# Kernel optimization log

Measured on AMD Instinct MI355X. Metric: run time of the kernel, lower is better.

The kernel has to match this reference:

```python
import jax, jax.numpy as jnp
import numpy as np

HIDDEN = 4096
N_HEADS = 32
N_KV_HEADS = 8
HEAD_SIZE = HIDDEN // N_HEADS  # 128
ROPE_THETA = 10000.0
SEQ_LEN = 1024
BATCH = 4


def setup_inputs() -> dict:
    key = jax.random.key(0)
    k1, k2, k3 = jax.random.split(key, 3)
    scale = 1.0 / np.sqrt(HIDDEN)
    hidden_states = jax.random.normal(k1, (BATCH * SEQ_LEN, HIDDEN), dtype=jnp.float32)
    w_qkv = jax.random.normal(k2, ((N_HEADS + 2 * N_KV_HEADS) * HEAD_SIZE, HIDDEN), dtype=jnp.float32) * scale
    w_o = jax.random.normal(k3, (HIDDEN, N_HEADS * HEAD_SIZE), dtype=jnp.float32) * scale
    return {"hidden_states": hidden_states, "w_qkv": w_qkv, "w_o": w_o, "seq_len": SEQ_LEN}


def _rope(x, pos, theta):
    # x: [B, S, H, D]; pos: [S] absolute positions; rotate-half (LLAMA/NeoX) style
    d = x.shape[-1]
    inv_freq = 1.0 / (theta ** (jnp.arange(0, d, 2, dtype=jnp.float32) / d))  # [D/2]
    ang = pos.astype(jnp.float32)[:, None] * inv_freq[None, :]  # [S, D/2]
    cos = jnp.cos(ang)[None, :, None, :]
    sin = jnp.sin(ang)[None, :, None, :]
    x1, x2 = jnp.split(x, 2, axis=-1)
    return jnp.concatenate([x1 * cos - x2 * sin, x2 * cos + x1 * sin], axis=-1)


def reference(hidden_states, w_qkv, w_o, seq_len):
    total, hidden = hidden_states.shape
    B = total // seq_len
    hd = HEAD_SIZE
    # fused QKV projection (bias-free), split like the torch module
    qkv = hidden_states @ w_qkv.T  # [T, (H+2K)*hd]
    q, k, v = jnp.split(qkv, [N_HEADS * hd, (N_HEADS + N_KV_HEADS) * hd], axis=1)
    q = q.reshape(B, seq_len, N_HEADS, hd)
    k = k.reshape(B, seq_len, N_KV_HEADS, hd)
    v = v.reshape(B, seq_len, N_KV_HEADS, hd)
    # inline RoPE (ROPE_LLAMA) on q and k at absolute positions
    pos = jnp.arange(seq_len)
    q = _rope(q, pos, ROPE_THETA)
    k = _rope(k, pos, ROPE_THETA)
    # GQA: map each q head to its kv head (kv_head_mapping = repeat_interleave)
    groups = N_HEADS // N_KV_HEADS
    k = jnp.repeat(k, groups, axis=2)  # [B, S, H, hd]
    v = jnp.repeat(v, groups, axis=2)
    scale = hd ** -0.5
    scores = jnp.einsum('bqhd,bkhd->bhqk', q, k) * scale  # [B, H, S, S]
    causal = jnp.tril(jnp.ones((seq_len, seq_len), dtype=bool))
    scores = jnp.where(causal[None, None], scores, jnp.finfo(scores.dtype).min)
    probs = jax.nn.softmax(scores, axis=-1)
    attn = jnp.einsum('bhqk,bkhd->bqhd', probs, v).reshape(total, N_HEADS * hd)
    return attn @ w_o.T  # [T, hidden]
```

## Files before the change

### kernel.cpp

```cpp
#include <hip/hip_runtime.h>


typedef short bf16x8 __attribute__((ext_vector_type(8)));
typedef short bf16x4 __attribute__((ext_vector_type(4)));
typedef float floatx4 __attribute__((ext_vector_type(4)));
typedef unsigned short u16x4 __attribute__((ext_vector_type(4)));

__device__ __forceinline__ unsigned short f2bf(float f) {
  unsigned u = __float_as_uint(f);
  u += 0x7FFFu + ((u >> 16) & 1u);
  return (unsigned short)(u >> 16);
}
__device__ __forceinline__ float bf2f(unsigned short h) {
  return __uint_as_float(((unsigned)h) << 16);
}

__device__ __forceinline__ void async16(const void* g, void* l) {
  __builtin_amdgcn_global_load_lds(
      (const __attribute__((address_space(1))) unsigned int*)g,
      (__attribute__((address_space(3))) unsigned int*)l, 16, 0, 0);
}

__global__ void cvt_f32_bf16(const float4* __restrict__ in,
                             u16x4* __restrict__ out, int n4) {
  int i = blockIdx.x * 256 + threadIdx.x;
  if (i < n4) {
    float4 v = in[i];
    u16x4 o;
    o.x = f2bf(v.x); o.y = f2bf(v.y); o.z = f2bf(v.z); o.w = f2bf(v.w);
    out[i] = o;
  }
}

template <int OUT_BF16>
__global__ __launch_bounds__(512, 2) void gemm256(
    const unsigned short* __restrict__ A, const unsigned short* __restrict__ B,
    void* __restrict__ Cout, int M, int N, int K) {
  __shared__ __align__(16) unsigned short As[4][8192];
  __shared__ __align__(16) unsigned short Bs[4][8192];
  const int tid = threadIdx.x;
  const int wave = tid >> 6, lane = tid & 63;
  const int wm = wave >> 2, wn = wave & 3;
  const int l16 = lane & 15, c4 = lane >> 4;
  const int bm = blockIdx.y << 8, bn = blockIdx.x << 8;

  int afOff[8], bfOff[4];
#pragma unroll
  for (int mi = 0; mi < 8; ++mi) {
    int r = wm * 128 + mi * 16 + l16;
    int pr = r >> 1, l8 = ((r & 1) << 2) | c4;
    afOff[mi] = pr * 128 + ((l8 ^ (pr & 7)) << 4);
  }
#pragma unroll
  for (int ni = 0; ni < 4; ++ni) {
    int r = wn * 64 + ni * 16 + l16;
    int pr = r >> 1, l8 = ((r & 1) << 2) | c4;
    bfOff[ni] = pr * 128 + ((l8 ^ (pr & 7)) << 4);
  }

  const int sp = lane >> 3;
  const int l8s = (lane & 7) ^ sp;
  const int so = l8s >> 2, sc = (l8s & 3) << 3;
  const unsigned short* aS0 = A + (size_t)(bm + wave * 16 + sp * 2 + so) * K + sc;
  const unsigned short* aS1 = A + (size_t)(bm + (wave + 8) * 16 + sp * 2 + so) * K + sc;
  const unsigned short* bS0 = B + (size_t)(bn + wave * 16 + sp * 2 + so) * K + sc;
  const unsigned short* bS1 = B + (size_t)(bn + (wave + 8) * 16 + sp * 2 + so) * K + sc;
  const int dst0 = wave * 1024, dst1 = (wave + 8) * 1024;

  floatx4 acc[8][4];
#pragma unroll
  for (int mi = 0; mi < 8; ++mi)
#pragma unroll
    for (int ni = 0; ni < 4; ++ni) acc[mi][ni] = (floatx4){0.f, 0.f, 0.f, 0.f};

  const int NT = K >> 5;
  async16(aS0, (char*)As[0] + dst0);
  async16(aS1, (char*)As[0] + dst1);
  async16(bS0, (char*)Bs[0] + dst0);
  async16(bS1, (char*)Bs[0] + dst1);
  async16(aS0 + 32, (char*)As[1] + dst0);
  async16(aS1 + 32, (char*)As[1] + dst1);
  async16(bS0 + 32, (char*)Bs[1] + dst0);
  async16(bS1 + 32, (char*)Bs[1] + dst1);
  asm volatile("s_waitcnt vmcnt(4)" ::: "memory");
  __builtin_amdgcn_s_barrier();

  size_t koff = 64;
  for (int t = 0; t < NT; ++t) {
    const char* aB = (const char*)As[t & 3];
    const char* bB = (const char*)Bs[t & 3];
    char* aD = (char*)As[(t + 2) & 3];
    char* bD = (char*)Bs[(t + 2) & 3];
    const bool st = (t + 2) < NT;

    bf16x8 af[8], bf[4];
#pragma unroll
    for (int mi = 0; mi < 4; ++mi) af[mi] = *(const bf16x8*)(aB + afOff[mi]);
#pragma unroll
    for (int ni = 0; ni < 4; ++ni) bf[ni] = *(const bf16x8*)(bB + bfOff[ni]);
    if (st) { async16(aS0 + koff, aD + dst0); async16(aS1 + koff, aD + dst1); }
    __builtin_amdgcn_s_barrier();
    __builtin_amdgcn_s_setprio(1);
#pragma unroll
    for (int mi = 0; mi < 4; ++mi)
#pragma unroll
      for (int ni = 0; ni < 4; ++ni)
        acc[mi][ni] = __builtin_amdgcn_mfma_f32_16x16x32_bf16(
            af[mi], bf[ni], acc[mi][ni], 0, 0, 0);
    __builtin_amdgcn_s_setprio(0);
    __builtin_amdgcn_s_barrier();

#pragma unroll
    for (int mi = 4; mi < 8; ++mi) af[mi] = *(const bf16x8*)(aB + afOff[mi]);
    if (st) { async16(bS0 + koff, bD + dst0); async16(bS1 + koff, bD + dst1); }
    __builtin_amdgcn_s_barrier();
    __builtin_amdgcn_s_setprio(1);
#pragma unroll
    for (int mi = 4; mi < 8; ++mi)
#pragma unroll
      for (int ni = 0; ni < 4; ++ni)
        acc[mi][ni] = __builtin_amdgcn_mfma_f32_16x16x32_bf16(
            af[mi], bf[ni], acc[mi][ni], 0, 0, 0);
    __builtin_amdgcn_s_setprio(0);
    if (st) asm volatile("s_waitcnt vmcnt(4)" ::: "memory");
    else    asm volatile("s_waitcnt vmcnt(0)" ::: "memory");
    __builtin_amdgcn_s_barrier();
    koff += 32;
  }

  const int col0 = bn + wn * 64 + l16;
#pragma unroll
  for (int mi = 0; mi < 8; ++mi) {
    const int row0 = bm + wm * 128 + mi * 16 + c4 * 4;
#pragma unroll
    for (int ni = 0; ni < 4; ++ni)
#pragma unroll
      for (int r = 0; r < 4; ++r) {
        if (OUT_BF16)
          ((unsigned short*)Cout)[(size_t)(row0 + r) * N + col0 + ni * 16] =
              f2bf(acc[mi][ni][r]);
        else
          ((float*)Cout)[(size_t)(row0 + r) * N + col0 + ni * 16] =
              acc[mi][ni][r];
      }
  }
}

__global__ void rope_k_kernel(unsigned short* __restrict__ qkv) {
  const int t = blockIdx.x;
  const int s = t & 1023;
  const int head = 32 + blockIdx.y * 4 + (threadIdx.x >> 6);
  const int d = threadIdx.x & 63;
  unsigned short* p = qkv + (size_t)t * 6144 + head * 128;
  float x1 = bf2f(p[d]), x2 = bf2f(p[d + 64]);
  float inv_freq = exp2f((float)d * -0.20762050593046015f);
  float ang = (float)s * inv_freq;
  float c, sn;
  __sincosf(ang, &sn, &c);
  p[d] = f2bf(x1 * c - x2 * sn);
  p[d + 64] = f2bf(x2 * c + x1 * sn);
}

__global__ __launch_bounds__(256, 3) void flash_attn(
    const unsigned short* __restrict__ qkv, unsigned short* __restrict__ aout) {
  const int pr = blockIdx.x;
  const int h = blockIdx.y, b = blockIdx.z;
  const int kh = h >> 2;
  const int tid = threadIdx.x;
  const int wave = tid >> 6, lane = tid & 63;
  const int quad = lane >> 4, l16 = lane & 15;

  __shared__ __align__(16) unsigned short Ks[64][136];
  __shared__ __align__(16) unsigned short Vt[128][68];
  __shared__ __align__(16) unsigned short Ps[64][68];

  const int krow = tid >> 4, kcol = (tid & 15) << 3;
  const int vrb = (tid & 15) << 2, vcol = (tid >> 4) << 3;
  const unsigned short* kp = qkv + (size_t)(b << 10) * 6144 + 4096 + kh * 128;
  const unsigned short* vp = qkv + (size_t)(b << 10) * 6144 + 5120 + kh * 128;

  for (int half = 0; half < 2; ++half) {
    const int qt = half ? pr : 15 - pr;
    const int q0 = qt << 6;

    bf16x8 qf[4];
    {
      const int qrow = q0 + wave * 16 + l16;
      const unsigned short* qp =
          qkv + (size_t)((b << 10) + qrow) * 6144 + h * 128 + quad * 8;
#pragma unroll
      for (int ks = 0; ks < 4; ++ks) qf[ks] = *(const bf16x8*)(qp + ks * 32);
      const float pos = (float)qrow;
      const float scale = 0.08838834764831845f;
#pragma unroll
      for (int ks = 0; ks < 2; ++ks)
#pragma unroll
        for (int e = 0; e < 8; ++e) {
          int d = ks * 32 + quad * 8 + e;
          float ang = pos * exp2f((float)d * -0.20762050593046015f);
          float c, sn;
          __sincosf(ang, &sn, &c);
          float x1 = bf2f((unsigned short)qf[ks][e]);
          float x2 = bf2f((unsigned short)qf[ks + 2][e]);
          qf[ks][e] = (short)f2bf((x1 * c - x2 * sn) * scale);
          qf[ks + 2][e] = (short)f2bf((x2 * c + x1 * sn) * scale);
        }
    }

    floatx4 o_acc[8];
#pragma unroll
    for (int i = 0; i < 8; ++i) o_acc[i] = (floatx4){0.f, 0.f, 0.f, 0.f};
    float l_lane[4] = {0.f, 0.f, 0.f, 0.f};

    bf16x8 kreg[4], vreg[4];
#pragma unroll
    for (int j = 0; j < 4; ++j)
      kreg[j] = *(const bf16x8*)(kp + (size_t)(krow + j * 16) * 6144 + kcol);
#pragma unroll
    for (int j = 0; j < 4; ++j)
      vreg[j] = *(const bf16x8*)(vp + (size_t)(vrb + j) * 6144 + vcol);

    for (int t = 0; t <= qt; ++t) {
      __syncthreads();
#pragma unroll
      for (int j = 0; j < 4; ++j)
        *(bf16x8*)&Ks[krow + j * 16][kcol] = kreg[j];
#pragma unroll
      for (int e = 0; e < 8; ++e) {
        bf16x4 w = {vreg[0][e], vreg[1][e], vreg[2][e], vreg[3][e]};
        *(bf16x4*)&Vt[vcol + e][vrb] = w;
      }
      __syncthreads();
      if (t < qt) {
        const size_t nb = (size_t)((t + 1) << 6) * 6144;
#pragma unroll
        for (int j = 0; j < 4; ++j)
          kreg[j] =
              *(const bf16x8*)(kp + nb + (size_t)(krow + j * 16) * 6144 + kcol);
#pragma unroll
        for (int j = 0; j < 4; ++j)
          vreg[j] = *(const bf16x8*)(vp + nb + (size_t)(vrb + j) * 6144 + vcol);
      }

      floatx4 sacc[4];
#pragma unroll
      for (int ni = 0; ni < 4; ++ni) sacc[ni] = (floatx4){0.f, 0.f, 0.f, 0.f};
#pragma unroll
      for (int ks = 0; ks < 4; ++ks)
#pragma unroll
        for (int ni = 0; ni < 4; ++ni) {
          bf16x8 kf = *(const bf16x8*)&Ks[ni * 16 + l16][ks * 32 + quad * 8];
          sacc[ni] = __builtin_amdgcn_mfma_f32_16x16x32_bf16(qf[ks], kf,
                                                             sacc[ni], 0, 0, 0);
        }

      const bool masked = (t == qt);
#pragma unroll
      for (int r = 0; r < 4; ++r) {
        float rs = 0.f;
#pragma unroll
        for (int ni = 0; ni < 4; ++ni) {
          float e = __expf(sacc[ni][r]);
          if (masked && (ni * 16 + l16) > (wave * 16 + quad * 4 + r)) e = 0.f;
          rs += e;
          Ps[wave * 16 + quad * 4 + r][ni * 16 + l16] = f2bf(e);
        }
        l_lane[r] += rs;
      }
      asm volatile("s_waitcnt lgkmcnt(0)" ::: "memory");

#pragma unroll
      for (int ks2 = 0; ks2 < 2; ++ks2) {
        bf16x8 pf = *(const bf16x8*)&Ps[wave * 16 + l16][ks2 * 32 + quad * 8];
#pragma unroll
        for (int n8 = 0; n8 < 8; ++n8) {
          bf16x8 vf = *(const bf16x8*)&Vt[n8 * 16 + l16][ks2 * 32 + quad * 8];
          o_acc[n8] = __builtin_amdgcn_mfma_f32_16x16x32_bf16(pf, vf, o_acc[n8],
                                                              0, 0, 0);
        }
      }
    }

#pragma unroll
    for (int r = 0; r < 4; ++r) {
      float l = l_lane[r];
#pragma unroll
      for (int off = 1; off < 16; off <<= 1) l += __shfl_xor(l, off, 64);
      float inv = 1.0f / l;
      int row = q0 + wave * 16 + quad * 4 + r;
      unsigned short* op = aout + (size_t)((b << 10) + row) * 4096 + h * 128;
#pragma unroll
      for (int n8 = 0; n8 < 8; ++n8)
        op[n8 * 16 + l16] = f2bf(o_acc[n8][r] * inv);
    }
  }
}

extern "C" void kernel_launch(void* const* d_in, const int* in_sizes, int n_in,
                              void* d_out, int out_size, void* d_ws,
                              size_t ws_size, hipStream_t stream) {
  const float* X = (const float*)d_in[0];
  const float* Wqkv = (const float*)d_in[1];
  const float* Wo = (const float*)d_in[2];
  (void)in_sizes; (void)n_in; (void)out_size; (void)ws_size;

  char* ws = (char*)d_ws;
  unsigned short* Wqkvb = (unsigned short*)ws;
  unsigned short* AttnB = (unsigned short*)ws;
  unsigned short* Xb = (unsigned short*)(ws + 50331648);
  unsigned short* Wob = (unsigned short*)(ws + 50331648);
  unsigned short* QKVb = (unsigned short*)(ws + 83886080);

  cvt_f32_bf16<<<16384, 256, 0, stream>>>((const float4*)X, (u16x4*)Xb, 4194304);
  cvt_f32_bf16<<<24576, 256, 0, stream>>>((const float4*)Wqkv, (u16x4*)Wqkvb, 6291456);
  gemm256<1><<<dim3(24, 16), 512, 0, stream>>>(Xb, Wqkvb, QKVb, 4096, 6144, 4096);
  rope_k_kernel<<<dim3(4096, 2), 256, 0, stream>>>(QKVb);
  cvt_f32_bf16<<<16384, 256, 0, stream>>>((const float4*)Wo, (u16x4*)Wob, 4194304);
  flash_attn<<<dim3(8, 32, 4), 256, 0, stream>>>(QKVb, AttnB);
  gemm256<0><<<dim3(16, 16), 512, 0, stream>>>(AttnB, Wob, d_out, 4096, 4096, 4096);
}
```

Before: 694.2 us.

## Prefetch next-tile LDS fragments into registers and remap blocks across XCDs

The K-loop of the bf16 GEMM is restructured so the next tile's first A half and its B fragments are read from LDS into double-buffered registers while the current MFMAs are still issuing. The loop is unrolled by two to ping-pong the B registers. Workgroup IDs are also remapped so consecutive tiles land on the same XCD, which should improve L2 reuse. In exchange, the stage guard is removed, so the last iterations issue async loads past K and read an unused LDS buffer. The loop also assumes an even tile count and a grid size divisible by 8.

```diff
diff --git a/kernel.cpp b/kernel.cpp
--- a/kernel.cpp
+++ b/kernel.cpp
@@ -42,7 +42,11 @@
   const int wave = tid >> 6, lane = tid & 63;
   const int wm = wave >> 2, wn = wave & 3;
   const int l16 = lane & 15, c4 = lane >> 4;
-  const int bm = blockIdx.y << 8, bn = blockIdx.x << 8;
+
+  const int nwg = gridDim.x * gridDim.y;
+  int bid = blockIdx.y * gridDim.x + blockIdx.x;
+  bid = (bid & 7) * (nwg >> 3) + (bid >> 3);
+  const int bm = (bid / gridDim.x) << 8, bn = (bid % gridDim.x) << 8;
 
   int afOff[8], bfOff[4];
 #pragma unroll
@@ -85,48 +89,58 @@
   asm volatile("s_waitcnt vmcnt(4)" ::: "memory");
   __builtin_amdgcn_s_barrier();
 
+  bf16x8 afq0[4], afq1[4], bfcA[4], bfcB[4];
+#pragma unroll
+  for (int i = 0; i < 4; ++i)
+    afq0[i] = *(const bf16x8*)((const char*)As[0] + afOff[i]);
+#pragma unroll
+  for (int i = 0; i < 4; ++i)
+    bfcA[i] = *(const bf16x8*)((const char*)Bs[0] + bfOff[i]);
+
   size_t koff = 64;
-  for (int t = 0; t < NT; ++t) {
-    const char* aB = (const char*)As[t & 3];
-    const char* bB = (const char*)Bs[t & 3];
-    char* aD = (char*)As[(t + 2) & 3];
-    char* bD = (char*)Bs[(t + 2) & 3];
-    const bool st = (t + 2) < NT;
-
-    bf16x8 af[8], bf[4];
-#pragma unroll
-    for (int mi = 0; mi < 4; ++mi) af[mi] = *(const bf16x8*)(aB + afOff[mi]);
-#pragma unroll
-    for (int ni = 0; ni < 4; ++ni) bf[ni] = *(const bf16x8*)(bB + bfOff[ni]);
-    if (st) { async16(aS0 + koff, aD + dst0); async16(aS1 + koff, aD + dst1); }
-    __builtin_amdgcn_s_barrier();
-    __builtin_amdgcn_s_setprio(1);
-#pragma unroll
-    for (int mi = 0; mi < 4; ++mi)
-#pragma unroll
-      for (int ni = 0; ni < 4; ++ni)
-        acc[mi][ni] = __builtin_amdgcn_mfma_f32_16x16x32_bf16(
-            af[mi], bf[ni], acc[mi][ni], 0, 0, 0);
-    __builtin_amdgcn_s_setprio(0);
-    __builtin_amdgcn_s_barrier();
-
-#pragma unroll
-    for (int mi = 4; mi < 8; ++mi) af[mi] = *(const bf16x8*)(aB + afOff[mi]);
-    if (st) { async16(bS0 + koff, bD + dst0); async16(bS1 + koff, bD + dst1); }
-    __builtin_amdgcn_s_barrier();
-    __builtin_amdgcn_s_setprio(1);
-#pragma unroll
-    for (int mi = 4; mi < 8; ++mi)
-#pragma unroll
-      for (int ni = 0; ni < 4; ++ni)
-        acc[mi][ni] = __builtin_amdgcn_mfma_f32_16x16x32_bf16(
-            af[mi], bf[ni], acc[mi][ni], 0, 0, 0);
-    __builtin_amdgcn_s_setprio(0);
-    if (st) asm volatile("s_waitcnt vmcnt(4)" ::: "memory");
-    else    asm volatile("s_waitcnt vmcnt(0)" ::: "memory");
-    __builtin_amdgcn_s_barrier();
-    koff += 32;
-  }
+
+#define KTILE(T, BC, BN_)                                                     \
+  {                                                                           \
+    const char* aB = (const char*)As[(T) & 3];                                \
+    const char* aN = (const char*)As[((T) + 1) & 3];                          \
+    const char* bN = (const char*)Bs[((T) + 1) & 3];                          \
+    char* aD = (char*)As[((T) + 2) & 3];                                      \
+    char* bD = (char*)Bs[((T) + 2) & 3];                                      \
+    _Pragma("unroll") for (int i = 0; i < 4; ++i)                             \
+        afq1[i] = *(const bf16x8*)(aB + afOff[4 + i]);                        \
+    async16(aS0 + koff, aD + dst0);                                           \
+    async16(aS1 + koff, aD + dst1);                                           \
+    __builtin_amdgcn_s_barrier();                                             \
+    __builtin_amdgcn_s_setprio(1);                                            \
+    _Pragma("unroll") for (int mi = 0; mi < 4; ++mi)                          \
+        _Pragma("unroll") for (int ni = 0; ni < 4; ++ni)                      \
+            acc[mi][ni] = __builtin_amdgcn_mfma_f32_16x16x32_bf16(            \
+                afq0[mi], BC[ni], acc[mi][ni], 0, 0, 0);                      \
+    __builtin_amdgcn_s_setprio(0);                                            \
+    asm volatile("s_waitcnt vmcnt(2)" ::: "memory");   \
+    __builtin_amdgcn_s_barrier();                     \
+    _Pragma("unroll") for (int i = 0; i < 4; ++i)                             \
+        afq0[i] = *(const bf16x8*)(aN + afOff[i]);                            \
+    _Pragma("unroll") for (int i = 0; i < 4; ++i)                             \
+        BN_[i] = *(const bf16x8*)(bN + bfOff[i]);                             \
+    async16(bS0 + koff, bD + dst0);                                           \
+    async16(bS1 + koff, bD + dst1);                                           \
+    __builtin_amdgcn_s_barrier();                                             \
+    __builtin_amdgcn_s_setprio(1);                                            \
+    _Pragma("unroll") for (int mi = 0; mi < 4; ++mi)                          \
+        _Pragma("unroll") for (int ni = 0; ni < 4; ++ni)                      \
+            acc[4 + mi][ni] = __builtin_amdgcn_mfma_f32_16x16x32_bf16(        \
+                afq1[mi], BC[ni], acc[4 + mi][ni], 0, 0, 0);                  \
+    __builtin_amdgcn_s_setprio(0);                                            \
+    __builtin_amdgcn_s_barrier();                                             \
+    koff += 32;                                                               \
+  }
+
+  for (int t = 0; t < NT; t += 2) {
+    KTILE(t, bfcA, bfcB);
+    KTILE(t + 1, bfcB, bfcA);
+  }
+#undef KTILE
 
   const int col0 = bn + wn * 64 + l16;
 #pragma unroll
```

Result: faster. 655.9 us (-5.5%).

## Prefetch next-tile LDS fragments in GEMM loop and fuse input conversions

Applied to the files above, without the earlier changes.

The GEMM main loop now software-pipelines LDS-to-register reads. The second half of the A fragments is loaded while the first MFMA batch runs, and the next tile's A/B fragments are loaded after the second batch, which cuts the barriers per k-step from three to two. Global-to-LDS prefetches are now issued unconditionally, so the final iterations read slightly past the K extent into tiles that are never consumed. Separately, the X and Wqkv fp32-to-bf16 conversions are merged into one launch to save a kernel launch.

```diff
diff --git a/kernel.cpp b/kernel.cpp
--- a/kernel.cpp
+++ b/kernel.cpp
@@ -19,6 +19,23 @@
   __builtin_amdgcn_global_load_lds(
       (const __attribute__((address_space(1))) unsigned int*)g,
       (__attribute__((address_space(3))) unsigned int*)l, 16, 0, 0);
+}
+
+__global__ void cvt_xw(const float4* __restrict__ X,
+                       const float4* __restrict__ Wq,
+                       u16x4* __restrict__ Xb, u16x4* __restrict__ Wqb) {
+  const float4* src;
+  u16x4* dst;
+  int j;
+  if (blockIdx.x < 16384) {
+    src = X; dst = Xb; j = blockIdx.x * 256 + threadIdx.x;
+  } else {
+    src = Wq; dst = Wqb; j = (blockIdx.x - 16384) * 256 + threadIdx.x;
+  }
+  float4 v = src[j];
+  u16x4 o;
+  o.x = f2bf(v.x); o.y = f2bf(v.y); o.z = f2bf(v.z); o.w = f2bf(v.w);
+  dst[j] = o;
 }
 
 __global__ void cvt_f32_bf16(const float4* __restrict__ in,
@@ -85,45 +102,54 @@
   asm volatile("s_waitcnt vmcnt(4)" ::: "memory");
   __builtin_amdgcn_s_barrier();
 
+  bf16x8 afq0[4], afq1[4], bfc[4];
+#pragma unroll
+  for (int i = 0; i < 4; ++i)
+    afq0[i] = *(const bf16x8*)((const char*)As[0] + afOff[i]);
+#pragma unroll
+  for (int i = 0; i < 4; ++i)
+    bfc[i] = *(const bf16x8*)((const char*)Bs[0] + bfOff[i]);
+
   size_t koff = 64;
   for (int t = 0; t < NT; ++t) {
-    const char* aB = (const char*)As[t & 3];
-    const char* bB = (const char*)Bs[t & 3];
-    char* aD = (char*)As[(t + 2) & 3];
-    char* bD = (char*)Bs[(t + 2) & 3];
-    const bool st = (t + 2) < NT;
-
-    bf16x8 af[8], bf[4];
-#pragma unroll
-    for (int mi = 0; mi < 4; ++mi) af[mi] = *(const bf16x8*)(aB + afOff[mi]);
-#pragma unroll
-    for (int ni = 0; ni < 4; ++ni) bf[ni] = *(const bf16x8*)(bB + bfOff[ni]);
-    if (st) { async16(aS0 + koff, aD + dst0); async16(aS1 + koff, aD + dst1); }
-    __builtin_amdgcn_s_barrier();
+    const char* aB = (const char*)As + ((size_t)(t & 3) << 14);
+    const char* aN = (const char*)As + ((size_t)((t + 1) & 3) << 14);
+    const char* bN = (const char*)Bs + ((size_t)((t + 1) & 3) << 14);
+    char* aD = (char*)As + ((size_t)((t + 2) & 3) << 14);
+    char* bD = (char*)Bs + ((size_t)((t + 2) & 3) << 14);
+
     __builtin_amdgcn_s_setprio(1);
 #pragma unroll
     for (int mi = 0; mi < 4; ++mi)
 #pragma unroll
       for (int ni = 0; ni < 4; ++ni)
         acc[mi][ni] = __builtin_amdgcn_mfma_f32_16x16x32_bf16(
-            af[mi], bf[ni], acc[mi][ni], 0, 0, 0);
+            afq0[mi], bfc[ni], acc[mi][ni], 0, 0, 0);
     __builtin_amdgcn_s_setprio(0);
+#pragma unroll
+    for (int i = 0; i < 4; ++i)
+      afq1[i] = *(const bf16x8*)(aB + afOff[4 + i]);
+    async16(aS0 + koff, aD + dst0);
+    async16(aS1 + koff, aD + dst1);
+    async16(bS0 + koff, bD + dst0);
+    async16(bS1 + koff, bD + dst1);
+    asm volatile("s_waitcnt vmcnt(4)" ::: "memory");
     __builtin_amdgcn_s_barrier();
 
-#pragma unroll
-    for (int mi = 4; mi < 8; ++mi) af[mi] = *(const bf16x8*)(aB + afOff[mi]);
-    if (st) { async16(bS0 + koff, bD + dst0); async16(bS1 + koff, bD + dst1); }
-    __builtin_amdgcn_s_barrier();
     __builtin_amdgcn_s_setprio(1);
 #pragma unroll
-    for (int mi = 4; mi < 8; ++mi)
+    for (int mi = 0; mi < 4; ++mi)
 #pragma unroll
       for (int ni = 0; ni < 4; ++ni)
-        acc[mi][ni] = __builtin_amdgcn_mfma_f32_16x16x32_bf16(
-            af[mi], bf[ni], acc[mi][ni], 0, 0, 0);
+        acc[4 + mi][ni] = __builtin_amdgcn_mfma_f32_16x16x32_bf16(
+            afq1[mi], bfc[ni], acc[4 + mi][ni], 0, 0, 0);
     __builtin_amdgcn_s_setprio(0);
-    if (st) asm volatile("s_waitcnt vmcnt(4)" ::: "memory");
-    else    asm volatile("s_waitcnt vmcnt(0)" ::: "memory");
+#pragma unroll
+    for (int i = 0; i < 4; ++i)
+      afq0[i] = *(const bf16x8*)(aN + afOff[i]);
+#pragma unroll
+    for (int i = 0; i < 4; ++i)
+      bfc[i] = *(const bf16x8*)(bN + bfOff[i]);
     __builtin_amdgcn_s_barrier();
     koff += 32;
   }
@@ -311,8 +337,8 @@
   unsigned short* Wob = (unsigned short*)(ws + 50331648);
   unsigned short* QKVb = (unsigned short*)(ws + 83886080);
 
-  cvt_f32_bf16<<<16384, 256, 0, stream>>>((const float4*)X, (u16x4*)Xb, 4194304);
-  cvt_f32_bf16<<<24576, 256, 0, stream>>>((const float4*)Wqkv, (u16x4*)Wqkvb, 6291456);
+  cvt_xw<<<40960, 256, 0, stream>>>((const float4*)X, (const float4*)Wqkv,
+                                    (u16x4*)Xb, (u16x4*)Wqkvb);
   gemm256<1><<<dim3(24, 16), 512, 0, stream>>>(Xb, Wqkvb, QKVb, 4096, 6144, 4096);
   rope_k_kernel<<<dim3(4096, 2), 256, 0, stream>>>(QKVb);
   cvt_f32_bf16<<<16384, 256, 0, stream>>>((const float4*)Wo, (u16x4*)Wob, 4194304);
```

Result: no change. 687.3 us (-1.0%).
